# Optimization experiments

Hardware: AMD Instinct MI355X
Metric: run time of the kernel (lower is better)

The kernel has to match this reference:

```python
import jax, jax.numpy as jnp
import numpy as np

N_ATOMS, N_NBH, N_IN, N_FILTERS, N_OUT, N_GAUSS = 10000, 48, 128, 128, 128, 25
R_CUTOFF = 5.0
LOG2 = float(np.log(2.0))


def ssp(v):
    # shifted softplus, the SchNet activation
    return jax.nn.softplus(v) - LOG2


def setup_inputs() -> dict:
    key = jax.random.key(0)
    ks = jax.random.split(key, 10)
    x = jax.random.normal(ks[0], (N_ATOMS, N_IN), dtype=jnp.float32)
    dR = jax.random.uniform(ks[1], (N_ATOMS, N_NBH), dtype=jnp.float32) * 10.0  # distances in [0,10)
    dR_expanded = jax.random.normal(ks[2], (N_ATOMS, N_NBH, N_GAUSS), dtype=jnp.float32)
    pairwise_mask = jnp.ones((N_ATOMS, N_NBH), dtype=jnp.float32)
    neighbors_idx = jax.random.randint(ks[3], (N_ATOMS, N_NBH), 0, N_ATOMS, dtype=jnp.int32)
    s = 1.0 / np.sqrt(N_FILTERS)
    W1 = jax.random.normal(ks[4], (N_GAUSS, N_FILTERS), dtype=jnp.float32) * (1.0 / np.sqrt(N_GAUSS))
    b1 = jnp.zeros((N_FILTERS,), dtype=jnp.float32)
    W2 = jax.random.normal(ks[5], (N_FILTERS, N_FILTERS), dtype=jnp.float32) * s
    b2 = jnp.zeros((N_FILTERS,), dtype=jnp.float32)
    W_in2f = jax.random.normal(ks[6], (N_IN, N_FILTERS), dtype=jnp.float32) * (1.0 / np.sqrt(N_IN))
    W_f2out = jax.random.normal(ks[7], (N_FILTERS, N_OUT), dtype=jnp.float32) * s
    b_f2out = jnp.zeros((N_OUT,), dtype=jnp.float32)
    return {"x": x, "dR": dR, "dR_expanded": dR_expanded, "pairwise_mask": pairwise_mask,
            "neighbors_idx": neighbors_idx, "W1": W1, "b1": b1, "W2": W2, "b2": b2,
            "W_in2f": W_in2f, "W_f2out": W_f2out, "b_f2out": b_f2out}


def reference(x, dR, dR_expanded, pairwise_mask, neighbors_idx,
              W1, b1, W2, b2, W_in2f, W_f2out, b_f2out):
    # FilterNetwork: Dense + ssp + Dense, on Gaussian-smeared distances -> [N, K, F]
    W = jnp.einsum('nkg,gf->nkf', dR_expanded, W1) + b1
    W = jnp.einsum('nkf,fh->nkh', ssp(W), W2) + b2
    # HardCutoff: 1 where within cutoff
    C = (dR <= R_CUTOFF).astype(W.dtype)           # [N, K]
    W = W * C[..., None]
    # in2f (no bias), gather neighbor features
    y = x @ W_in2f                                  # [N, F]
    y = jnp.take(y, neighbors_idx, axis=0)          # [N, K, F] (gather == take_along_axis path)
    # filter-weighted multiply + masked sum aggregation over neighbor axis
    y = y * W
    y = jnp.sum(y * pairwise_mask[..., None], axis=1)  # [N, F]
    # f2out: Linear + shifted softplus
    return ssp(y @ W_f2out + b_f2out)               # [N, n_out]
```

## Files before the change

### kernel.cpp

```cpp
#include <hip/hip_runtime.h>
#include <hip/hip_bf16.h>


#define NA 10000
#define NK 48
#define NF 128
#define DREP 40
#define HP   136

typedef __bf16 bf16x8 __attribute__((ext_vector_type(8)));
typedef float  f32x4  __attribute__((ext_vector_type(4)));

__device__ __forceinline__ unsigned short f2bs(float x) {
    return __builtin_bit_cast(unsigned short, (__bf16)x);
}
__device__ __forceinline__ float bs2f(unsigned short u) {
    return (float)__builtin_bit_cast(__bf16, u);
}
__device__ __forceinline__ float sspf(float v) {
    return fmaxf(v, 0.0f) + __logf(1.0f + __expf(-fabsf(v))) - 0.69314718056f;
}

__global__ __launch_bounds__(256) void prep_weights(
    const float* __restrict__ W1,
    const float* __restrict__ W2,
    const float* __restrict__ Wi,
    unsigned short* __restrict__ wsb)
{
    int i = blockIdx.x * 256 + threadIdx.x;
    if (i < 4096) {
        int f = i >> 5, g = i & 31;
        wsb[i] = (g < 25) ? f2bs(W1[g * NF + f]) : (unsigned short)0;
    } else if (i < 20480) {
        int j = i - 4096; int h = j >> 7, k = j & 127;
        wsb[i] = f2bs(W2[k * NF + h]);
    } else if (i < 36864) {
        int j = i - 20480; int f = j >> 7, k = j & 127;
        wsb[i] = f2bs(Wi[k * NF + f]);
    }
}

__global__ __launch_bounds__(256) void in2f_mfma(
    const float* __restrict__ x,
    const unsigned short* __restrict__ WiT,
    unsigned short* __restrict__ yfeatb)
{
    const int tid = threadIdx.x;
    const int w = tid >> 6;
    const int lane = tid & 63;
    const int r = lane & 15;
    const int q = lane >> 4;
    const int m0 = blockIdx.x * 64 + w * 16;
    const int row = m0 + r;
    const bool rv = (row < NA);

    f32x4 acc[8];
    #pragma unroll
    for (int nt = 0; nt < 8; ++nt) { acc[nt][0]=0.f; acc[nt][1]=0.f; acc[nt][2]=0.f; acc[nt][3]=0.f; }

    #pragma unroll
    for (int ks = 0; ks < 4; ++ks) {
        bf16x8 a;
        if (rv) {
            const float4* xp = (const float4*)(x + (size_t)row * NF + ks * 32 + q * 8);
            float4 v0 = xp[0], v1 = xp[1];
            a[0]=(__bf16)v0.x; a[1]=(__bf16)v0.y; a[2]=(__bf16)v0.z; a[3]=(__bf16)v0.w;
            a[4]=(__bf16)v1.x; a[5]=(__bf16)v1.y; a[6]=(__bf16)v1.z; a[7]=(__bf16)v1.w;
        } else {
            #pragma unroll
            for (int j = 0; j < 8; ++j) a[j] = (__bf16)0.0f;
        }
        #pragma unroll
        for (int nt = 0; nt < 8; ++nt) {
            bf16x8 b = *(const bf16x8*)(WiT + (nt * 16 + r) * NF + ks * 32 + q * 8);
            acc[nt] = __builtin_amdgcn_mfma_f32_16x16x32_bf16(a, b, acc[nt], 0, 0, 0);
        }
    }
    #pragma unroll
    for (int nt = 0; nt < 8; ++nt) {
        #pragma unroll
        for (int reg = 0; reg < 4; ++reg) {
            int orow = m0 + q * 4 + reg;
            if (orow < NA)
                yfeatb[(size_t)orow * NF + nt * 16 + r] = f2bs(acc[nt][reg]);
        }
    }
}

__global__ __launch_bounds__(256) void cfconv_mfma(
    const float* __restrict__ dR,
    const float* __restrict__ dRe,
    const float* __restrict__ mask,
    const int*   __restrict__ nbr,
    const float* __restrict__ b1,
    const float* __restrict__ b2,
    const float* __restrict__ Wf2o,
    const float* __restrict__ bf2o,
    const unsigned short* __restrict__ W1T,
    const unsigned short* __restrict__ W2T,
    const unsigned short* __restrict__ yfeatb,
    float* __restrict__ out)
{
    __shared__ __align__(16) unsigned short s_dre[NK * DREP];
    __shared__ __align__(16) unsigned short s_H[NK * HP];
    __shared__ __align__(16) float s_y[NF];
    __shared__ __align__(16) float s_part[256];
    __shared__ float s_cm[NK];
    __shared__ int   s_nb[NK];

    const int tid = threadIdx.x;
    const int n = blockIdx.x;
    const int w = tid >> 6;
    const int lane = tid & 63;
    const int r = lane & 15;
    const int q = lane >> 4;
    const int nt0 = w * 2;

    {
        unsigned int* z = (unsigned int*)s_dre;
        for (int i = tid; i < NK * DREP / 2; i += 256) z[i] = 0u;
    }
    if (tid < NK) {
        float d = dR[n * NK + tid];
        float m = mask[n * NK + tid];
        s_cm[tid] = (d <= 5.0f) ? m : 0.0f;
        s_nb[tid] = nbr[n * NK + tid] * NF;
    }
    __syncthreads();
    {
        const float* dre = dRe + (size_t)n * (NK * 25);
        for (int i = tid; i < NK * 25; i += 256) {
            int k = i / 25;
            int g = i - k * 25;
            s_dre[k * DREP + g] = f2bs(dre[i]);
        }
    }
    __syncthreads();

    const float bias1a = b1[nt0 * 16 + r];
    const float bias1b = b1[nt0 * 16 + 16 + r];
    {
        bf16x8 bfr[2];
        bfr[0] = *(const bf16x8*)(W1T + ((nt0    ) * 16 + r) * 32 + q * 8);
        bfr[1] = *(const bf16x8*)(W1T + ((nt0 + 1) * 16 + r) * 32 + q * 8);
        #pragma unroll
        for (int mt = 0; mt < 3; ++mt) {
            bf16x8 a = *(const bf16x8*)(&s_dre[(mt * 16 + r) * DREP + q * 8]);
            #pragma unroll
            for (int t = 0; t < 2; ++t) {
                f32x4 zf; zf[0]=0.f; zf[1]=0.f; zf[2]=0.f; zf[3]=0.f;
                f32x4 h = __builtin_amdgcn_mfma_f32_16x16x32_bf16(a, bfr[t], zf, 0, 0, 0);
                float bia = t ? bias1b : bias1a;
                #pragma unroll
                for (int reg = 0; reg < 4; ++reg) {
                    int k = mt * 16 + q * 4 + reg;
                    int f = (nt0 + t) * 16 + r;
                    s_H[k * HP + f] = f2bs(sspf(h[reg] + bia));
                }
            }
        }
    }
    __syncthreads();

    const float bias2a = b2[nt0 * 16 + r];
    const float bias2b = b2[nt0 * 16 + 16 + r];
    f32x4 acc[3][2];
    #pragma unroll
    for (int mt = 0; mt < 3; ++mt)
        #pragma unroll
        for (int t = 0; t < 2; ++t) { acc[mt][t][0]=0.f; acc[mt][t][1]=0.f; acc[mt][t][2]=0.f; acc[mt][t][3]=0.f; }

    bf16x8 bw[2][4];
    #pragma unroll
    for (int t = 0; t < 2; ++t)
        #pragma unroll
        for (int ks = 0; ks < 4; ++ks)
            bw[t][ks] = *(const bf16x8*)(W2T + ((nt0 + t) * 16 + r) * NF + ks * 32 + q * 8);

    #pragma unroll
    for (int ks = 0; ks < 4; ++ks) {
        #pragma unroll
        for (int mt = 0; mt < 3; ++mt) {
            bf16x8 a = *(const bf16x8*)(&s_H[(mt * 16 + r) * HP + ks * 32 + q * 8]);
            #pragma unroll
            for (int t = 0; t < 2; ++t)
                acc[mt][t] = __builtin_amdgcn_mfma_f32_16x16x32_bf16(a, bw[t][ks], acc[mt][t], 0, 0, 0);
        }
    }

    float part0 = 0.f, part1 = 0.f;
    const int h0 = nt0 * 16 + r;
    #pragma unroll
    for (int mt = 0; mt < 3; ++mt) {
        #pragma unroll
        for (int reg = 0; reg < 4; ++reg) {
            int k = mt * 16 + q * 4 + reg;
            float cmk = s_cm[k];
            int base = s_nb[k];
            part0 += cmk * (acc[mt][0][reg] + bias2a) * bs2f(yfeatb[base + h0]);
            part1 += cmk * (acc[mt][1][reg] + bias2b) * bs2f(yfeatb[base + h0 + 16]);
        }
    }
    part0 += __shfl_xor(part0, 16);
    part0 += __shfl_xor(part0, 32);
    part1 += __shfl_xor(part1, 16);
    part1 += __shfl_xor(part1, 32);
    if (q == 0) {
        s_y[h0] = part0;
        s_y[h0 + 16] = part1;
    }
    __syncthreads();

    {
        int f = tid & 127;
        int half = tid >> 7;
        float o = 0.f;
        const float* wp = Wf2o + (size_t)(half * 64) * NF + f;
        const float* yp = s_y + half * 64;
        #pragma unroll 8
        for (int i = 0; i < 64; ++i)
            o = fmaf(yp[i], wp[(size_t)i * NF], o);
        s_part[tid] = o;
    }
    __syncthreads();
    if (tid < NF)
        out[(size_t)n * NF + tid] = sspf(s_part[tid] + s_part[tid + 128] + bf2o[tid]);
}

extern "C" void kernel_launch(void* const* d_in, const int* in_sizes, int n_in,
                              void* d_out, int out_size, void* d_ws, size_t ws_size,
                              hipStream_t stream)
{
    const float* x    = (const float*)d_in[0];
    const float* dR   = (const float*)d_in[1];
    const float* dRe  = (const float*)d_in[2];
    const float* mask = (const float*)d_in[3];
    const int*   nbr  = (const int*)d_in[4];
    const float* W1   = (const float*)d_in[5];
    const float* b1   = (const float*)d_in[6];
    const float* W2   = (const float*)d_in[7];
    const float* b2   = (const float*)d_in[8];
    const float* Wi2f = (const float*)d_in[9];
    const float* Wf2o = (const float*)d_in[10];
    const float* bf2o = (const float*)d_in[11];
    float* out = (float*)d_out;

    unsigned short* wsb = (unsigned short*)d_ws;
    unsigned short* W1T    = wsb;
    unsigned short* W2T    = wsb + 4096;
    unsigned short* WiT    = wsb + 20480;
    unsigned short* yfeatb = wsb + 36864;

    prep_weights<<<144, 256, 0, stream>>>(W1, W2, Wi2f, wsb);
    in2f_mfma<<<157, 256, 0, stream>>>(x, WiT, yfeatb);
    cfconv_mfma<<<NA, 256, 0, stream>>>(dR, dRe, mask, nbr, b1, b2, Wf2o, bf2o,
                                        W1T, W2T, yfeatb, out);
}
```

Before: 201.8 us.

## Split f2out into separate MFMA kernel and prefetch neighbor features into LDS

The per-atom cfconv kernel no longer does the scalar f2out GEMV. It now writes aggregated features to the output buffer, and a new batched MFMA kernel applies the f2out linear layer and softplus in place. The neighbor gathers, weight fragments and the Gaussian-expanded distances are loaded up front straight into registers. This removes the LDS staging pass and two barriers, and gathered rows are kept in LDS for the reduction. The cost is an extra launch, a round trip of the intermediate through global memory, and f2out inputs rounded to bf16.

```diff
diff --git a/kernel.cpp b/kernel.cpp
--- a/kernel.cpp
+++ b/kernel.cpp
@@ -5,8 +5,8 @@
 #define NA 10000
 #define NK 48
 #define NF 128
-#define DREP 40
-#define HP   136
+#define HP  136
+#define YFP 136
 
 typedef __bf16 bf16x8 __attribute__((ext_vector_type(8)));
 typedef float  f32x4  __attribute__((ext_vector_type(4)));
@@ -25,6 +25,7 @@
     const float* __restrict__ W1,
     const float* __restrict__ W2,
     const float* __restrict__ Wi,
+    const float* __restrict__ Wo,
     unsigned short* __restrict__ wsb)
 {
     int i = blockIdx.x * 256 + threadIdx.x;
@@ -37,6 +38,9 @@
     } else if (i < 36864) {
         int j = i - 20480; int f = j >> 7, k = j & 127;
         wsb[i] = f2bs(Wi[k * NF + f]);
+    } else if (i < 53248) {
+        int j = i - 36864; int f = j >> 7, k = j & 127;
+        wsb[i] = f2bs(Wo[k * NF + f]);
     }
 }
 
@@ -94,19 +98,14 @@
     const int*   __restrict__ nbr,
     const float* __restrict__ b1,
     const float* __restrict__ b2,
-    const float* __restrict__ Wf2o,
-    const float* __restrict__ bf2o,
     const unsigned short* __restrict__ W1T,
     const unsigned short* __restrict__ W2T,
     const unsigned short* __restrict__ yfeatb,
-    float* __restrict__ out)
-{
-    __shared__ __align__(16) unsigned short s_dre[NK * DREP];
+    float* __restrict__ yout)
+{
     __shared__ __align__(16) unsigned short s_H[NK * HP];
-    __shared__ __align__(16) float s_y[NF];
-    __shared__ __align__(16) float s_part[256];
+    __shared__ __align__(16) unsigned short s_yf[NK * YFP];
     __shared__ float s_cm[NK];
-    __shared__ int   s_nb[NK];
 
     const int tid = threadIdx.x;
     const int n = blockIdx.x;
@@ -116,75 +115,80 @@
     const int q = lane >> 4;
     const int nt0 = w * 2;
 
-    {
-        unsigned int* z = (unsigned int*)s_dre;
-        for (int i = tid; i < NK * DREP / 2; i += 256) z[i] = 0u;
-    }
+    const int kb = tid >> 4;
+    const int sp = tid & 15;
+    const int nb0 = nbr[n * NK + kb] * NF;
+    const int nb1 = nbr[n * NK + kb + 16] * NF;
+    const int nb2 = nbr[n * NK + kb + 32] * NF;
+    bf16x8 g0 = *(const bf16x8*)(yfeatb + nb0 + sp * 8);
+    bf16x8 g1 = *(const bf16x8*)(yfeatb + nb1 + sp * 8);
+    bf16x8 g2 = *(const bf16x8*)(yfeatb + nb2 + sp * 8);
+
+    bf16x8 bfr0 = *(const bf16x8*)(W1T + ((nt0    ) * 16 + r) * 32 + q * 8);
+    bf16x8 bfr1 = *(const bf16x8*)(W1T + ((nt0 + 1) * 16 + r) * 32 + q * 8);
+    bf16x8 bw[2][4];
+    #pragma unroll
+    for (int t = 0; t < 2; ++t)
+        #pragma unroll
+        for (int ks = 0; ks < 4; ++ks)
+            bw[t][ks] = *(const bf16x8*)(W2T + ((nt0 + t) * 16 + r) * NF + ks * 32 + q * 8);
+
     if (tid < NK) {
         float d = dR[n * NK + tid];
         float m = mask[n * NK + tid];
         s_cm[tid] = (d <= 5.0f) ? m : 0.0f;
-        s_nb[tid] = nbr[n * NK + tid] * NF;
-    }
-    __syncthreads();
-    {
-        const float* dre = dRe + (size_t)n * (NK * 25);
-        for (int i = tid; i < NK * 25; i += 256) {
-            int k = i / 25;
-            int g = i - k * 25;
-            s_dre[k * DREP + g] = f2bs(dre[i]);
-        }
-    }
-    __syncthreads();
+    }
 
     const float bias1a = b1[nt0 * 16 + r];
     const float bias1b = b1[nt0 * 16 + 16 + r];
-    {
-        bf16x8 bfr[2];
-        bfr[0] = *(const bf16x8*)(W1T + ((nt0    ) * 16 + r) * 32 + q * 8);
-        bfr[1] = *(const bf16x8*)(W1T + ((nt0 + 1) * 16 + r) * 32 + q * 8);
-        #pragma unroll
-        for (int mt = 0; mt < 3; ++mt) {
-            bf16x8 a = *(const bf16x8*)(&s_dre[(mt * 16 + r) * DREP + q * 8]);
-            #pragma unroll
-            for (int t = 0; t < 2; ++t) {
-                f32x4 zf; zf[0]=0.f; zf[1]=0.f; zf[2]=0.f; zf[3]=0.f;
-                f32x4 h = __builtin_amdgcn_mfma_f32_16x16x32_bf16(a, bfr[t], zf, 0, 0, 0);
-                float bia = t ? bias1b : bias1a;
-                #pragma unroll
-                for (int reg = 0; reg < 4; ++reg) {
-                    int k = mt * 16 + q * 4 + reg;
-                    int f = (nt0 + t) * 16 + r;
-                    s_H[k * HP + f] = f2bs(sspf(h[reg] + bia));
-                }
-            }
-        }
-    }
-    __syncthreads();
-
     const float bias2a = b2[nt0 * 16 + r];
     const float bias2b = b2[nt0 * 16 + 16 + r];
+
+    const float* dre_n = dRe + (size_t)n * (NK * 25);
+    #pragma unroll
+    for (int mt = 0; mt < 3; ++mt) {
+        bf16x8 a;
+        if (q < 3) {
+            float av[8];
+            __builtin_memcpy(av, dre_n + (mt * 16 + r) * 25 + q * 8, 32);
+            #pragma unroll
+            for (int j = 0; j < 8; ++j) a[j] = (__bf16)av[j];
+        } else {
+            float v = dre_n[(mt * 16 + r) * 25 + 24];
+            a[0] = (__bf16)v;
+            #pragma unroll
+            for (int j = 1; j < 8; ++j) a[j] = (__bf16)0.0f;
+        }
+        f32x4 zf; zf[0]=0.f; zf[1]=0.f; zf[2]=0.f; zf[3]=0.f;
+        f32x4 h0v = __builtin_amdgcn_mfma_f32_16x16x32_bf16(a, bfr0, zf, 0, 0, 0);
+        f32x4 h1v = __builtin_amdgcn_mfma_f32_16x16x32_bf16(a, bfr1, zf, 0, 0, 0);
+        #pragma unroll
+        for (int reg = 0; reg < 4; ++reg) {
+            int k = mt * 16 + q * 4 + reg;
+            s_H[k * HP + nt0 * 16 + r]      = f2bs(sspf(h0v[reg] + bias1a));
+            s_H[k * HP + nt0 * 16 + 16 + r] = f2bs(sspf(h1v[reg] + bias1b));
+        }
+    }
+
+    *(bf16x8*)(&s_yf[(kb     ) * YFP + sp * 8]) = g0;
+    *(bf16x8*)(&s_yf[(kb + 16) * YFP + sp * 8]) = g1;
+    *(bf16x8*)(&s_yf[(kb + 32) * YFP + sp * 8]) = g2;
+
+    __syncthreads();
+
     f32x4 acc[3][2];
     #pragma unroll
     for (int mt = 0; mt < 3; ++mt)
         #pragma unroll
         for (int t = 0; t < 2; ++t) { acc[mt][t][0]=0.f; acc[mt][t][1]=0.f; acc[mt][t][2]=0.f; acc[mt][t][3]=0.f; }
-
-    bf16x8 bw[2][4];
-    #pragma unroll
-    for (int t = 0; t < 2; ++t)
-        #pragma unroll
-        for (int ks = 0; ks < 4; ++ks)
-            bw[t][ks] = *(const bf16x8*)(W2T + ((nt0 + t) * 16 + r) * NF + ks * 32 + q * 8);
 
     #pragma unroll
     for (int ks = 0; ks < 4; ++ks) {
         #pragma unroll
         for (int mt = 0; mt < 3; ++mt) {
             bf16x8 a = *(const bf16x8*)(&s_H[(mt * 16 + r) * HP + ks * 32 + q * 8]);
-            #pragma unroll
-            for (int t = 0; t < 2; ++t)
-                acc[mt][t] = __builtin_amdgcn_mfma_f32_16x16x32_bf16(a, bw[t][ks], acc[mt][t], 0, 0, 0);
+            acc[mt][0] = __builtin_amdgcn_mfma_f32_16x16x32_bf16(a, bw[0][ks], acc[mt][0], 0, 0, 0);
+            acc[mt][1] = __builtin_amdgcn_mfma_f32_16x16x32_bf16(a, bw[1][ks], acc[mt][1], 0, 0, 0);
         }
     }
 
@@ -196,9 +200,8 @@
         for (int reg = 0; reg < 4; ++reg) {
             int k = mt * 16 + q * 4 + reg;
             float cmk = s_cm[k];
-            int base = s_nb[k];
-            part0 += cmk * (acc[mt][0][reg] + bias2a) * bs2f(yfeatb[base + h0]);
-            part1 += cmk * (acc[mt][1][reg] + bias2b) * bs2f(yfeatb[base + h0 + 16]);
+            part0 += cmk * (acc[mt][0][reg] + bias2a) * bs2f(s_yf[k * YFP + h0]);
+            part1 += cmk * (acc[mt][1][reg] + bias2b) * bs2f(s_yf[k * YFP + h0 + 16]);
         }
     }
     part0 += __shfl_xor(part0, 16);
@@ -206,25 +209,57 @@
     part1 += __shfl_xor(part1, 16);
     part1 += __shfl_xor(part1, 32);
     if (q == 0) {
-        s_y[h0] = part0;
-        s_y[h0 + 16] = part1;
-    }
-    __syncthreads();
-
-    {
-        int f = tid & 127;
-        int half = tid >> 7;
-        float o = 0.f;
-        const float* wp = Wf2o + (size_t)(half * 64) * NF + f;
-        const float* yp = s_y + half * 64;
-        #pragma unroll 8
-        for (int i = 0; i < 64; ++i)
-            o = fmaf(yp[i], wp[(size_t)i * NF], o);
-        s_part[tid] = o;
-    }
-    __syncthreads();
-    if (tid < NF)
-        out[(size_t)n * NF + tid] = sspf(s_part[tid] + s_part[tid + 128] + bf2o[tid]);
+        yout[(size_t)n * NF + h0]      = part0;
+        yout[(size_t)n * NF + h0 + 16] = part1;
+    }
+}
+
+__global__ __launch_bounds__(256) void f2out_mfma(
+    const unsigned short* __restrict__ WoT,
+    const float* __restrict__ bo,
+    float* io)
+{
+    const int tid = threadIdx.x;
+    const int w = tid >> 6;
+    const int lane = tid & 63;
+    const int r = lane & 15;
+    const int q = lane >> 4;
+    const int m0 = blockIdx.x * 64 + w * 16;
+    const int row = m0 + r;
+    const bool rv = (row < NA);
+
+    f32x4 acc[8];
+    #pragma unroll
+    for (int nt = 0; nt < 8; ++nt) { acc[nt][0]=0.f; acc[nt][1]=0.f; acc[nt][2]=0.f; acc[nt][3]=0.f; }
+
+    #pragma unroll
+    for (int ks = 0; ks < 4; ++ks) {
+        bf16x8 a;
+        if (rv) {
+            const float4* yp = (const float4*)(io + (size_t)row * NF + ks * 32 + q * 8);
+            float4 v0 = yp[0], v1 = yp[1];
+            a[0]=(__bf16)v0.x; a[1]=(__bf16)v0.y; a[2]=(__bf16)v0.z; a[3]=(__bf16)v0.w;
+            a[4]=(__bf16)v1.x; a[5]=(__bf16)v1.y; a[6]=(__bf16)v1.z; a[7]=(__bf16)v1.w;
+        } else {
+            #pragma unroll
+            for (int j = 0; j < 8; ++j) a[j] = (__bf16)0.0f;
+        }
+        #pragma unroll
+        for (int nt = 0; nt < 8; ++nt) {
+            bf16x8 b = *(const bf16x8*)(WoT + (nt * 16 + r) * NF + ks * 32 + q * 8);
+            acc[nt] = __builtin_amdgcn_mfma_f32_16x16x32_bf16(a, b, acc[nt], 0, 0, 0);
+        }
+    }
+    #pragma unroll
+    for (int nt = 0; nt < 8; ++nt) {
+        float bia = bo[nt * 16 + r];
+        #pragma unroll
+        for (int reg = 0; reg < 4; ++reg) {
+            int orow = m0 + q * 4 + reg;
+            if (orow < NA)
+                io[(size_t)orow * NF + nt * 16 + r] = sspf(acc[nt][reg] + bia);
+        }
+    }
 }
 
 extern "C" void kernel_launch(void* const* d_in, const int* in_sizes, int n_in,
@@ -249,10 +284,12 @@
     unsigned short* W1T    = wsb;
     unsigned short* W2T    = wsb + 4096;
     unsigned short* WiT    = wsb + 20480;
-    unsigned short* yfeatb = wsb + 36864;
-
-    prep_weights<<<144, 256, 0, stream>>>(W1, W2, Wi2f, wsb);
+    unsigned short* WoT    = wsb + 36864;
+    unsigned short* yfeatb = wsb + 53248;
+
+    prep_weights<<<208, 256, 0, stream>>>(W1, W2, Wi2f, Wf2o, wsb);
     in2f_mfma<<<157, 256, 0, stream>>>(x, WiT, yfeatb);
-    cfconv_mfma<<<NA, 256, 0, stream>>>(dR, dRe, mask, nbr, b1, b2, Wf2o, bf2o,
+    cfconv_mfma<<<NA, 256, 0, stream>>>(dR, dRe, mask, nbr, b1, b2,
                                         W1T, W2T, yfeatb, out);
-}
+    f2out_mfma<<<157, 256, 0, stream>>>(WoT, bf2o, out);
+}
```

New measurement: 198.4 us. About the same (-1.7%).
